# Kernel tuning notes

Measured on AMD Instinct MI355X. Metric: run time of the kernel, lower is better.

## Reference

```python
import jax, jax.numpy as jnp
import numpy as np

B, S, E = 4, 2048, 1024
HIDDEN = 1024
HEADS = 16


def setup_inputs() -> dict:
    key = jax.random.key(0)
    k0, k1, k2, k3, k4 = jax.random.split(key, 5)
    inputs = jax.random.normal(k0, (B, S, E), dtype=jnp.float32)
    W_qkv = jax.random.normal(k1, (E, 3 * HIDDEN), dtype=jnp.float32) * 0.02
    b_qkv = jnp.zeros((3 * HIDDEN,), dtype=jnp.float32)
    W_out = jax.random.normal(k2, (HIDDEN, HIDDEN), dtype=jnp.float32) * 0.02
    b_out = jnp.zeros((HIDDEN,), dtype=jnp.float32)
    return {"inputs": inputs, "W_qkv": W_qkv, "b_qkv": b_qkv, "W_out": W_out, "b_out": b_out}


def reference(inputs, W_qkv, b_qkv, W_out, b_out):
    Bv, Sv, Ev = inputs.shape
    x = inputs @ W_qkv + b_qkv                      # [B, S, 3*hidden]
    # Faithful to the original: reshape mixes seq and hidden exactly as the source does.
    x = x.reshape(Bv, HEADS, Sv, -1)                # [B, H, S, 3*hidden/H]
    q, k, v = jnp.split(x, 3, axis=-1)              # each [B, H, S, hidden/H]
    scale = (2 * HIDDEN) ** (-0.5)
    qk = jnp.einsum('bhse,bhte->bhst', q, k) * scale  # [B, H, S, S]
    mask = jnp.triu(jnp.full((Sv, Sv), -jnp.inf, dtype=qk.dtype), k=1)
    attn = jax.nn.softmax(qk + mask, axis=-1)
    sa = jnp.einsum('bhst,bhte->bhse', attn, v).reshape(Bv, Sv, -1)  # [B, S, hidden]
    return sa @ W_out + b_out
```

## Files before the change

### kernel.cpp

```cpp
#include <hip/hip_runtime.h>
#include <hip/hip_bf16.h>

using bf16 = __hip_bfloat16;

typedef __attribute__((ext_vector_type(8))) short short8;
typedef __attribute__((ext_vector_type(4))) float f32x4;


#define CEXP 0.03188127742677263f

__device__ __forceinline__ unsigned short f2bf(float v) {
  bf16 h = __float2bfloat16(v);
  return *(unsigned short*)&h;
}
__device__ __forceinline__ unsigned int pack2bf(float a, float b) {
  return (unsigned int)f2bf(a) | ((unsigned int)f2bf(b) << 16);
}

__device__ __forceinline__ void gload_lds16(const void* g, void* lds) {
  __builtin_amdgcn_global_load_lds(
      (const __attribute__((address_space(1))) unsigned int*)(g),
      (__attribute__((address_space(3))) unsigned int*)(lds), 16, 0, 0);
}

__global__ void detect_kernel(const unsigned int* __restrict__ x, int* __restrict__ flag) {
  unsigned int w = x[threadIdx.x];
  unsigned int e = (w >> 7) & 0xFF;
  bool inband = (e >= 96 && e <= 133);
  unsigned long long m = __ballot(inband);
  if (threadIdx.x == 0) flag[0] = (__popcll(m) >= 48) ? 0 : 1;
}

__global__ __launch_bounds__(256) void convert_kernel(
    const void* __restrict__ src, bf16* __restrict__ dst, int n8,
    const int* __restrict__ flag) {
  int i = blockIdx.x * 256 + threadIdx.x;
  if (i >= n8) return;
  uint4 outv;
  if (*flag) {
    const float4* s = (const float4*)src + (size_t)i * 2;
    float4 a = s[0], b = s[1];
    outv.x = pack2bf(a.x, a.y);
    outv.y = pack2bf(a.z, a.w);
    outv.z = pack2bf(b.x, b.y);
    outv.w = pack2bf(b.z, b.w);
  } else {
    outv = ((const uint4*)src)[i];
  }
  ((uint4*)dst)[i] = outv;
}

__global__ void convert_bias_qkv(const void* __restrict__ src, bf16* __restrict__ dst,
                                 const int* __restrict__ flag) {
  int i = blockIdx.x * 256 + threadIdx.x;
  if (i >= 3072) return;
  float v = (*flag) ? ((const float*)src)[i]
                    : __bfloat162float(((const bf16*)src)[i]);
  if ((i % 192) < 64) v *= CEXP;
  dst[i] = __float2bfloat16(v);
}

__global__ __launch_bounds__(256) void transpose_bf16(
    const void* __restrict__ src, bf16* __restrict__ dst, int R, int Cc,
    const int* __restrict__ flag, int qscale) {
  __shared__ float tile[32][33];
  const int c0 = blockIdx.x * 32, r0 = blockIdx.y * 32;
  const int tx = threadIdx.x & 31, ty = threadIdx.x >> 5;
  const bool f32 = (*flag != 0);
#pragma unroll
  for (int it = 0; it < 4; ++it) {
    int r = ty + it * 8;
    float v;
    if (f32) v = ((const float*)src)[(size_t)(r0 + r) * Cc + c0 + tx];
    else     v = __bfloat162float(((const bf16*)src)[(size_t)(r0 + r) * Cc + c0 + tx]);
    tile[r][tx] = v;
  }
  __syncthreads();
#pragma unroll
  for (int it = 0; it < 4; ++it) {
    int r = ty + it * 8;
    float vv = tile[tx][r];
    if (qscale && (((c0 + r) % 192) < 64)) vv *= CEXP;
    dst[(size_t)(c0 + r) * R + r0 + tx] = __float2bfloat16(vv);
  }
}

__global__ __launch_bounds__(256) void transpose_v(const bf16* __restrict__ qkv,
                                                   bf16* __restrict__ vtg)
{
  __shared__ short tile[64][72];
  const int bh = blockIdx.x;
  const int k0 = blockIdx.y * 64;
  const unsigned short* qk = (const unsigned short*)qkv + (size_t)bh * 393216;
  const int key = threadIdx.x & 63;
  const int dv = threadIdx.x >> 6;
  const int gk = k0 + key;
  const unsigned short* src =
      qk + (size_t)(gk >> 4) * 3072 + (gk & 15) * 192 + 128 + dv * 16;
  *(short8*)&tile[key][dv * 16] = *(const short8*)src;
  *(short8*)&tile[key][dv * 16 + 8] = *(const short8*)(src + 8);
  __syncthreads();
  const int d = threadIdx.x & 63;
  const int kv = threadIdx.x >> 6;
  unsigned short* dst =
      (unsigned short*)vtg + ((size_t)bh * 64 + d) * 2048 + k0 + kv * 16;
  short8 a, b;
#pragma unroll
  for (int j = 0; j < 8; ++j) {
    a[j] = tile[kv * 16 + j][d];
    b[j] = tile[kv * 16 + 8 + j][d];
  }
  *(short8*)dst = a;
  *(short8*)(dst + 8) = b;
}

__global__ __launch_bounds__(256) void gemm128(
    const bf16* __restrict__ A, const bf16* __restrict__ BT,
    const bf16* __restrict__ bias, void* __restrict__ C,
    int M, int N, int K, int store_mode, const int* __restrict__ flag)
{
  __shared__ alignas(16) short As2[2][8192];
  __shared__ alignas(16) short Bs2[2][8192];
  const bool store_f32 = store_mode && (*flag != 0);
  const int tid = threadIdx.x;
  const int lane = tid & 63;
  const int w = tid >> 6;
  const int l15 = lane & 15, l4 = lane >> 4;
  const int wm2 = w >> 1, wn4 = w & 1;

  const int nwg = gridDim.x * gridDim.y;
  const int orig = blockIdx.x + gridDim.x * blockIdx.y;
  const int qn = nwg >> 3;
  const int swz = (orig & 7) * qn + (orig >> 3);
  const int bx = swz % gridDim.x, by = swz / gridDim.x;
  const int m0 = by * 128, n0 = bx * 128;

  const int srow = tid >> 3;
  const int koff = ((tid & 7) ^ (srow & 7)) << 3;
  const bf16* pa = A + (size_t)(m0 + srow) * K + koff;
  const bf16* pb = BT + (size_t)(n0 + srow) * K + koff;
  const int dst0 = tid * 8;

  const int rsw = l15 & 7;

  f32x4 acc[4][4] = {};
  const int nt = K >> 6;

#pragma unroll
  for (int q = 0; q < 4; ++q) {
    gload_lds16(pa + (size_t)(q * 32) * K, &As2[0][q * 2048 + dst0]);
    gload_lds16(pb + (size_t)(q * 32) * K, &Bs2[0][q * 2048 + dst0]);
  }

  for (int t = 0; t < nt; ++t) {
    const int c = t & 1;
    if (t + 1 < nt) {
      const int nb = c ^ 1;
      const bf16* sa_ = pa + (size_t)(t + 1) * 64;
      const bf16* sb_ = pb + (size_t)(t + 1) * 64;
#pragma unroll
      for (int q = 0; q < 4; ++q) {
        gload_lds16(sa_ + (size_t)(q * 32) * K, &As2[nb][q * 2048 + dst0]);
        gload_lds16(sb_ + (size_t)(q * 32) * K, &Bs2[nb][q * 2048 + dst0]);
      }
      asm volatile("s_waitcnt vmcnt(8)" ::: "memory");
    } else {
      asm volatile("s_waitcnt vmcnt(0)" ::: "memory");
    }
    __builtin_amdgcn_s_barrier();
    asm volatile("" ::: "memory");

#pragma unroll
    for (int s = 0; s < 2; ++s) {
      const int cgs = (((s << 2) | l4) ^ rsw) * 8;
      short8 af[4], bfr[4];
#pragma unroll
      for (int i = 0; i < 4; ++i)
        af[i] = *(const short8*)&As2[c][(wm2 * 64 + i * 16 + l15) * 64 + cgs];
#pragma unroll
      for (int j = 0; j < 4; ++j)
        bfr[j] = *(const short8*)&Bs2[c][(wn4 * 64 + j * 16 + l15) * 64 + cgs];
      __builtin_amdgcn_s_setprio(1);
#pragma unroll
      for (int i = 0; i < 4; ++i)
#pragma unroll
        for (int j = 0; j < 4; ++j)
          acc[i][j] = __builtin_amdgcn_mfma_f32_16x16x32_bf16(af[i], bfr[j], acc[i][j], 0, 0, 0);
      __builtin_amdgcn_s_setprio(0);
    }
    asm volatile("" ::: "memory");
    __builtin_amdgcn_s_barrier();
    asm volatile("" ::: "memory");
  }

#pragma unroll
  for (int j = 0; j < 4; ++j) {
    const int n = n0 + wn4 * 64 + j * 16 + l15;
    const float bv = __bfloat162float(bias[n]);
#pragma unroll
    for (int i = 0; i < 4; ++i) {
#pragma unroll
      for (int r = 0; r < 4; ++r) {
        const int mrow = m0 + wm2 * 64 + i * 16 + l4 * 4 + r;
        const float v = acc[i][j][r] + bv;
        if (store_f32) ((float*)C)[(size_t)mrow * N + n] = v;
        else           ((bf16*)C)[(size_t)mrow * N + n] = __float2bfloat16(v);
      }
    }
  }
}

__global__ __launch_bounds__(512) void attn_mfma(const bf16* __restrict__ qkv,
                                                 const bf16* __restrict__ vtg,
                                                 bf16* __restrict__ sa)
{
  __shared__ alignas(16) short Ks[2][4096];
  __shared__ alignas(16) short Vs[2][4096];
  __shared__ alignas(16) short Ps[8][1152];
  const int tid = threadIdx.x;
  const int bh = blockIdx.x;
  const int pr = blockIdx.y;
  const size_t base = (size_t)bh * 393216;
  const int w = tid >> 6;
  const int g = w >> 2;
  const int wl = w & 3;
  const int lane = tid & 63;
  const int l15 = lane & 15, l4 = lane >> 4;
  const unsigned short* qk = (const unsigned short*)qkv;
  const unsigned short* vtb = (const unsigned short*)vtg + (size_t)bh * 131072;
  short* psw = &Ps[w][0];

  const int qc = g ? pr : (15 - pr);
  const int my_ktmax  = 2 * qc + 1;
  const int blk_ktmax = 2 * (15 - pr) + 1;

  const unsigned short* gsrc0 =
      g ? (vtb + (size_t)lane * 2048)
        : (qk + base + (size_t)(lane >> 4) * 3072 + (lane & 15) * 192 + 64);
  const size_t gstep = g ? 64 : 12288;

  short8 qf[2][2];
#pragma unroll
  for (int h = 0; h < 2; ++h) {
    const unsigned short* pq =
        qk + base + (size_t)(qc * 8 + 2 * wl + h) * 3072 + l15 * 192 + l4 * 8;
    qf[h][0] = *(const short8*)pq;
    qf[h][1] = *(const short8*)(pq + 32);
  }

  f32x4 o[2][4] = {};
  float ml[2] = {-__builtin_inff(), -__builtin_inff()};
  float ls[2] = {0.f, 0.f};
  int cur = 0;

  {
    short* dstbuf = g ? &Vs[0][0] : &Ks[0][0];
    gload_lds16(gsrc0 + wl * 8, dstbuf + wl * 512);
    gload_lds16(gsrc0 + (wl + 4) * 8, dstbuf + (wl + 4) * 512);
  }
  __syncthreads();

  for (int kt = 0; kt <= blk_ktmax; ++kt) {
    if (kt < blk_ktmax) {
      short* dstbuf = g ? &Vs[cur ^ 1][0] : &Ks[cur ^ 1][0];
      const unsigned short* s = gsrc0 + (size_t)(kt + 1) * gstep;
      gload_lds16(s + wl * 8, dstbuf + wl * 512);
      gload_lds16(s + (wl + 4) * 8, dstbuf + (wl + 4) * 512);
    }

    if (kt <= my_ktmax) {
      f32x4 sc[2][4];
#pragma unroll
      for (int t = 0; t < 4; ++t) {
        const short8 kf0 = *(const short8*)&Ks[cur][(l4) * 512 + (16 * t + l15) * 8];
        const short8 kf1 = *(const short8*)&Ks[cur][(4 + l4) * 512 + (16 * t + l15) * 8];
#pragma unroll
        for (int h = 0; h < 2; ++h) {
          f32x4 c = {};
          c = __builtin_amdgcn_mfma_f32_16x16x32_bf16(kf0, qf[h][0], c, 0, 0, 0);
          c = __builtin_amdgcn_mfma_f32_16x16x32_bf16(kf1, qf[h][1], c, 0, 0, 0);
          sc[h][t] = c;
        }
      }

      if (kt >= 2 * qc) {
        const int kb = 64 * (kt - 2 * qc);
#pragma unroll
        for (int h = 0; h < 2; ++h) {
          const int thr = 32 * wl + 16 * h + l15;
#pragma unroll
          for (int t = 0; t < 4; ++t)
#pragma unroll
            for (int r = 0; r < 4; ++r)
              if (kb + 16 * t + 4 * l4 + r > thr) sc[h][t][r] = -__builtin_inff();
        }
      }

      unsigned int pk2[2][4][2];
#pragma unroll
      for (int h = 0; h < 2; ++h) {
        float mx = -__builtin_inff();
#pragma unroll
        for (int t = 0; t < 4; ++t)
#pragma unroll
          for (int r = 0; r < 4; ++r) mx = fmaxf(mx, sc[h][t][r]);
        mx = fmaxf(mx, __shfl_xor(mx, 16, 64));
        mx = fmaxf(mx, __shfl_xor(mx, 32, 64));
        if (!__all(mx <= ml[h] + 8.f)) {
          const float m_new = fmaxf(ml[h], mx);
          const float alpha = __builtin_amdgcn_exp2f(ml[h] - m_new);
          ml[h] = m_new;
          ls[h] *= alpha;
#pragma unroll
          for (int jn = 0; jn < 4; ++jn)
#pragma unroll
            for (int r = 0; r < 4; ++r) o[h][jn][r] *= alpha;
        }
        const float m_new = ml[h];
        float s = 0.f;
#pragma unroll
        for (int t = 0; t < 4; ++t) {
          float p0 = __builtin_amdgcn_exp2f(sc[h][t][0] - m_new);
          float p1 = __builtin_amdgcn_exp2f(sc[h][t][1] - m_new);
          float p2 = __builtin_amdgcn_exp2f(sc[h][t][2] - m_new);
          float p3 = __builtin_amdgcn_exp2f(sc[h][t][3] - m_new);
          s += (p0 + p1) + (p2 + p3);
          pk2[h][t][0] = pack2bf(p0, p1);
          pk2[h][t][1] = pack2bf(p2, p3);
        }
        s += __shfl_xor(s, 16, 64);
        s += __shfl_xor(s, 32, 64);
        ls[h] += s;
      }

      short8 pf[2][2];
#pragma unroll
      for (int h = 0; h < 2; ++h) {
#pragma unroll
        for (int t = 0; t < 4; ++t) {
          uint2 wv; wv.x = pk2[h][t][0]; wv.y = pk2[h][t][1];
          *(uint2*)(psw + l15 * 72 + 16 * t + 4 * l4) = wv;
        }
        pf[h][0] = *(const short8*)(psw + l15 * 72 + 8 * l4);
        pf[h][1] = *(const short8*)(psw + l15 * 72 + 32 + 8 * l4);
      }

#pragma unroll
      for (int jn = 0; jn < 4; ++jn)
#pragma unroll
        for (int ks = 0; ks < 2; ++ks) {
          const short8 vf =
              *(const short8*)&Vs[cur][(4 * ks + l4) * 512 + (16 * jn + l15) * 8];
#pragma unroll
          for (int h = 0; h < 2; ++h)
            o[h][jn] = __builtin_amdgcn_mfma_f32_16x16x32_bf16(vf, pf[h][ks], o[h][jn], 0, 0, 0);
        }
    }

    __syncthreads();
    cur ^= 1;
  }

#pragma unroll
  for (int h = 0; h < 2; ++h) {
    const float inv = 1.0f / ls[h];
    unsigned short* so =
        (unsigned short*)sa + (size_t)(bh * 128 + qc * 8 + 2 * wl + h) * 1024;
#pragma unroll
    for (int jn = 0; jn < 4; ++jn) {
      uint2 wv;
      wv.x = pack2bf(o[h][jn][0] * inv, o[h][jn][1] * inv);
      wv.y = pack2bf(o[h][jn][2] * inv, o[h][jn][3] * inv);
      *(uint2*)(so + l15 * 64 + jn * 16 + l4 * 4) = wv;
    }
  }
}

extern "C" void kernel_launch(void* const* d_in, const int* in_sizes, int n_in,
                              void* d_out, int out_size, void* d_ws, size_t ws_size,
                              hipStream_t stream)
{
  const void* x_raw    = d_in[0];
  const void* Wqkv_raw = d_in[1];
  const void* bqkv_raw = d_in[2];
  const void* Wout_raw = d_in[3];
  const void* bout_raw = d_in[4];

  char* ws = (char*)d_ws;
  int*  flag   = (int*)ws;
  bf16* xb     = (bf16*)(ws + 256);
  bf16* wqkvT  = xb + (size_t)8192 * 1024;
  bf16* bqkvb  = wqkvT + (size_t)3072 * 1024;
  bf16* woutT  = bqkvb + 4096;
  bf16* boutb  = woutT + (size_t)1024 * 1024;
  bf16* qkv    = boutb + 4096;
  bf16* sa     = qkv + (size_t)8192 * 3072;
  bf16* vtg    = sa + (size_t)8192 * 1024;

  detect_kernel<<<1, 64, 0, stream>>>((const unsigned int*)x_raw, flag);

  convert_kernel<<<(8192 * 1024 / 8 + 255) / 256, 256, 0, stream>>>(x_raw, xb, 8192 * 1024 / 8, flag);
  convert_bias_qkv<<<12, 256, 0, stream>>>(bqkv_raw, bqkvb, flag);
  convert_kernel<<<1, 256, 0, stream>>>(bout_raw, boutb, 1024 / 8, flag);
  transpose_bf16<<<dim3(3072 / 32, 1024 / 32), 256, 0, stream>>>(Wqkv_raw, wqkvT, 1024, 3072, flag, 1);
  transpose_bf16<<<dim3(1024 / 32, 1024 / 32), 256, 0, stream>>>(Wout_raw, woutT, 1024, 1024, flag, 0);

  gemm128<<<dim3(3072 / 128, 8192 / 128), 256, 0, stream>>>(
      xb, wqkvT, bqkvb, qkv, 8192, 3072, 1024, 0, flag);
  transpose_v<<<dim3(64, 32), 256, 0, stream>>>(qkv, vtg);
  attn_mfma<<<dim3(64, 8), 512, 0, stream>>>(qkv, vtg, sa);
  gemm128<<<dim3(1024 / 128, 8192 / 128), 256, 0, stream>>>(
      sa, woutT, boutb, d_out, 8192, 1024, 1024, 1, flag);
}
```

Before: 270.3 us.

## Fuse V transpose into QKV GEMM epilogue and merge bias conversions

Measured after the change: 292.4 us. 1.08x slower.

```diff
diff --git a/kernel.cpp b/kernel.cpp
--- a/kernel.cpp
+++ b/kernel.cpp
@@ -50,14 +50,24 @@
   ((uint4*)dst)[i] = outv;
 }
 
-__global__ void convert_bias_qkv(const void* __restrict__ src, bf16* __restrict__ dst,
-                                 const int* __restrict__ flag) {
+__global__ void convert_biases(const void* __restrict__ bqkv_src,
+                               const void* __restrict__ bout_src,
+                               bf16* __restrict__ bqkv_dst,
+                               bf16* __restrict__ bout_dst,
+                               const int* __restrict__ flag) {
   int i = blockIdx.x * 256 + threadIdx.x;
-  if (i >= 3072) return;
-  float v = (*flag) ? ((const float*)src)[i]
-                    : __bfloat162float(((const bf16*)src)[i]);
-  if ((i % 192) < 64) v *= CEXP;
-  dst[i] = __float2bfloat16(v);
+  const bool f32 = (*flag != 0);
+  if (i < 3072) {
+    float v = f32 ? ((const float*)bqkv_src)[i]
+                  : __bfloat162float(((const bf16*)bqkv_src)[i]);
+    if ((i % 192) < 64) v *= CEXP;
+    bqkv_dst[i] = __float2bfloat16(v);
+  } else if (i < 4096) {
+    int j = i - 3072;
+    float v = f32 ? ((const float*)bout_src)[j]
+                  : __bfloat162float(((const bf16*)bout_src)[j]);
+    bout_dst[j] = __float2bfloat16(v);
+  }
 }
 
 __global__ __launch_bounds__(256) void transpose_bf16(
@@ -85,38 +95,10 @@
   }
 }
 
-__global__ __launch_bounds__(256) void transpose_v(const bf16* __restrict__ qkv,
-                                                   bf16* __restrict__ vtg)
-{
-  __shared__ short tile[64][72];
-  const int bh = blockIdx.x;
-  const int k0 = blockIdx.y * 64;
-  const unsigned short* qk = (const unsigned short*)qkv + (size_t)bh * 393216;
-  const int key = threadIdx.x & 63;
-  const int dv = threadIdx.x >> 6;
-  const int gk = k0 + key;
-  const unsigned short* src =
-      qk + (size_t)(gk >> 4) * 3072 + (gk & 15) * 192 + 128 + dv * 16;
-  *(short8*)&tile[key][dv * 16] = *(const short8*)src;
-  *(short8*)&tile[key][dv * 16 + 8] = *(const short8*)(src + 8);
-  __syncthreads();
-  const int d = threadIdx.x & 63;
-  const int kv = threadIdx.x >> 6;
-  unsigned short* dst =
-      (unsigned short*)vtg + ((size_t)bh * 64 + d) * 2048 + k0 + kv * 16;
-  short8 a, b;
-#pragma unroll
-  for (int j = 0; j < 8; ++j) {
-    a[j] = tile[kv * 16 + j][d];
-    b[j] = tile[kv * 16 + 8 + j][d];
-  }
-  *(short8*)dst = a;
-  *(short8*)(dst + 8) = b;
-}
-
 __global__ __launch_bounds__(256) void gemm128(
     const bf16* __restrict__ A, const bf16* __restrict__ BT,
     const bf16* __restrict__ bias, void* __restrict__ C,
+    bf16* __restrict__ vt_out,
     int M, int N, int K, int store_mode, const int* __restrict__ flag)
 {
   __shared__ alignas(16) short As2[2][8192];
@@ -197,6 +179,11 @@
   for (int j = 0; j < 4; ++j) {
     const int n = n0 + wn4 * 64 + j * 16 + l15;
     const float bv = __bfloat162float(bias[n]);
+    const int rq = n / 192;
+    const int c192 = n - rq * 192;
+    const bool isV = (vt_out != nullptr) && (c192 >= 128);
+    unsigned short* vvb =
+        (unsigned short*)vt_out + (((size_t)(c192 - 128)) << 11) + rq;
 #pragma unroll
     for (int i = 0; i < 4; ++i) {
 #pragma unroll
@@ -205,6 +192,10 @@
         const float v = acc[i][j][r] + bv;
         if (store_f32) ((float*)C)[(size_t)mrow * N + n] = v;
         else           ((bf16*)C)[(size_t)mrow * N + n] = __float2bfloat16(v);
+        if (isV) {
+          const int bh = mrow >> 7, u = mrow & 127;
+          vvb[((size_t)bh << 17) + (u << 4)] = f2bf(v);
+        }
       }
     }
   }
@@ -216,7 +207,7 @@
 {
   __shared__ alignas(16) short Ks[2][4096];
   __shared__ alignas(16) short Vs[2][4096];
-  __shared__ alignas(16) short Ps[8][1152];
+  __shared__ alignas(16) short Ps[8][2304];
   const int tid = threadIdx.x;
   const int bh = blockIdx.x;
   const int pr = blockIdx.y;
@@ -333,17 +324,19 @@
         ls[h] += s;
       }
 
-      short8 pf[2][2];
-#pragma unroll
-      for (int h = 0; h < 2; ++h) {
+#pragma unroll
+      for (int h = 0; h < 2; ++h)
 #pragma unroll
         for (int t = 0; t < 4; ++t) {
           uint2 wv; wv.x = pk2[h][t][0]; wv.y = pk2[h][t][1];
-          *(uint2*)(psw + l15 * 72 + 16 * t + 4 * l4) = wv;
-        }
-        pf[h][0] = *(const short8*)(psw + l15 * 72 + 8 * l4);
-        pf[h][1] = *(const short8*)(psw + l15 * 72 + 32 + 8 * l4);
-      }
+          *(uint2*)(psw + (16 * h + l15) * 72 + 16 * t + 4 * l4) = wv;
+        }
+      short8 pf[2][2];
+#pragma unroll
+      for (int h = 0; h < 2; ++h)
+#pragma unroll
+        for (int ks = 0; ks < 2; ++ks)
+          pf[h][ks] = *(const short8*)(psw + (16 * h + l15) * 72 + 32 * ks + 8 * l4);
 
 #pragma unroll
       for (int jn = 0; jn < 4; ++jn)
@@ -400,15 +393,13 @@
   detect_kernel<<<1, 64, 0, stream>>>((const unsigned int*)x_raw, flag);
 
   convert_kernel<<<(8192 * 1024 / 8 + 255) / 256, 256, 0, stream>>>(x_raw, xb, 8192 * 1024 / 8, flag);
-  convert_bias_qkv<<<12, 256, 0, stream>>>(bqkv_raw, bqkvb, flag);
-  convert_kernel<<<1, 256, 0, stream>>>(bout_raw, boutb, 1024 / 8, flag);
+  convert_biases<<<16, 256, 0, stream>>>(bqkv_raw, bout_raw, bqkvb, boutb, flag);
   transpose_bf16<<<dim3(3072 / 32, 1024 / 32), 256, 0, stream>>>(Wqkv_raw, wqkvT, 1024, 3072, flag, 1);
   transpose_bf16<<<dim3(1024 / 32, 1024 / 32), 256, 0, stream>>>(Wout_raw, woutT, 1024, 1024, flag, 0);
 
   gemm128<<<dim3(3072 / 128, 8192 / 128), 256, 0, stream>>>(
-      xb, wqkvT, bqkvb, qkv, 8192, 3072, 1024, 0, flag);
-  transpose_v<<<dim3(64, 32), 256, 0, stream>>>(qkv, vtg);
+      xb, wqkvT, bqkvb, qkv, vtg, 8192, 3072, 1024, 0, flag);
   attn_mfma<<<dim3(64, 8), 512, 0, stream>>>(qkv, vtg, sa);
   gemm128<<<dim3(1024 / 128, 8192 / 128), 256, 0, stream>>>(
-      sa, woutT, boutb, d_out, 8192, 1024, 1024, 1, flag);
-}
+      sa, woutT, boutb, d_out, nullptr, 8192, 1024, 1024, 1, flag);
+}
```
